# Kernel tuning notes

Hardware: AMD Instinct MI355X
Metric: run time of the kernel (lower is better)

## Reference

```python
import jax, jax.numpy as jnp
import numpy as np

B, N, DIM, IN_DIM, H = 8, 3136, 147, 64, 1
HD = IN_DIM // H          # per-head value/key dim = 64
MLP_HID = int(IN_DIM * 1.0)
EPS = 1e-5


def _ln(x, w, b):
    m = jnp.mean(x, axis=-1, keepdims=True)
    v = jnp.mean((x - m) ** 2, axis=-1, keepdims=True)
    return (x - m) / jnp.sqrt(v + EPS) * w + b


def setup_inputs() -> dict:
    key = jax.random.key(0)
    ks = jax.random.split(key, 12)
    r = lambda k, shp, s=0.02: (jax.random.normal(k, shp, dtype=jnp.float32) * s)
    return {
        "x": jax.random.normal(ks[0], (B, N, DIM), dtype=jnp.float32),
        "norm1_w": jnp.ones((DIM,), jnp.float32),
        "norm1_b": jnp.zeros((DIM,), jnp.float32),
        "qkv_w": r(ks[1], (3 * IN_DIM, DIM)),
        "scale": jnp.full((H,), (DIM // H) ** -0.5, dtype=jnp.float32),
        "proj_w": r(ks[2], (IN_DIM, IN_DIM)),
        "proj_b": jnp.zeros((IN_DIM,), jnp.float32),
        "norm2_w": jnp.ones((IN_DIM,), jnp.float32),
        "norm2_b": jnp.zeros((IN_DIM,), jnp.float32),
        "fc1_w": r(ks[3], (MLP_HID, IN_DIM)),
        "fc1_b": jnp.zeros((MLP_HID,), jnp.float32),
        "fc2_w": r(ks[4], (IN_DIM, MLP_HID)),
        "fc2_b": jnp.zeros((IN_DIM,), jnp.float32),
    }


def reference(x, norm1_w, norm1_b, qkv_w, scale, proj_w, proj_b,
              norm2_w, norm2_b, fc1_w, fc1_b, fc2_w, fc2_b):
    h = _ln(x, norm1_w, norm1_b)                               # [B,N,DIM]
    qkv = jnp.einsum('bnc,oc->bno', h, qkv_w)                  # [B,N,3*IN_DIM]
    qkv = qkv.reshape(B, N, 3, H, HD).transpose(2, 0, 3, 1, 4)  # [3,B,H,N,HD]
    q, k, v = qkv[0], qkv[1], qkv[2]
    # LMSA: learnable per-head scale + diagonal (self) exclusion mask
    attn = jnp.einsum('bhid,bhjd->bhij', q, k) * scale[None, :, None, None]
    eye = jnp.eye(N, dtype=bool)
    attn = jnp.where(eye[None, None], -jnp.inf, attn)
    attn = jax.nn.softmax(attn, axis=-1)
    o = jnp.einsum('bhij,bhjd->bhid', attn, v)                 # [B,H,N,HD]
    o = o.transpose(0, 2, 1, 3).reshape(B, N, IN_DIM)
    o = jnp.einsum('bnd,od->bno', o, proj_w) + proj_b
    # num_heads == 1 -> residual is v itself
    x_attn = v[:, 0] + o                                       # [B,N,IN_DIM]
    h2 = _ln(x_attn, norm2_w, norm2_b)
    h2 = jax.nn.gelu(jnp.einsum('bnd,hd->bnh', h2, fc1_w) + fc1_b,
                     approximate=False)
    h2 = jnp.einsum('bnh,oh->bno', h2, fc2_w) + fc2_b
    return x_attn + h2
```

## Files before the change

kernel.cpp:

```cpp
#include <hip/hip_runtime.h>
#include <math.h>
#include <stdint.h>

#define B_    8
#define N_    3136
#define DIM_  147
#define KP_   160
#define TOK_  (B_*N_)
#define QKV3_ 192
#define NSPLIT 4

typedef __attribute__((ext_vector_type(4)))  float f32x4;
typedef __attribute__((ext_vector_type(16))) float f32x16;
typedef __attribute__((ext_vector_type(4)))  unsigned int u32x4;
typedef __attribute__((ext_vector_type(2)))  unsigned int u32x2;
typedef __attribute__((ext_vector_type(8)))  short short8;
typedef float f32x4u __attribute__((ext_vector_type(4), aligned(4)));
typedef union { short8 s; u32x4 u; } pk8;

static __device__ __forceinline__ unsigned short f2b(float f){
  unsigned int u = __float_as_uint(f);
  u += 0x7fffu + ((u>>16)&1u);
  return (unsigned short)(u>>16);
}
static __device__ __forceinline__ unsigned int pk2(float a, float b){
  return ((unsigned int)f2b(b)<<16) | (unsigned int)f2b(a);
}
static __device__ __forceinline__ unsigned int pk2t(float a, float b){
  return (__float_as_uint(b) & 0xffff0000u) | (__float_as_uint(a)>>16);
}
static __device__ __forceinline__ float b2f(unsigned short s){
  return __uint_as_float(((unsigned int)s)<<16);
}

#define GLD16(gp, lp) __builtin_amdgcn_global_load_lds( \
    reinterpret_cast<const uint32_t __attribute__((address_space(1)))*>(reinterpret_cast<uintptr_t>(gp)), \
    reinterpret_cast<uint32_t __attribute__((address_space(3)))*>(reinterpret_cast<uintptr_t>(lp)), \
    16, 0, 0)

__global__ __launch_bounds__(256) void k_qkv(const float* __restrict__ x,
                                             const float* __restrict__ w1,
                                             const float* __restrict__ b1,
                                             const float* __restrict__ qkvw,
                                             const float* __restrict__ scale,
                                             unsigned short* __restrict__ qb,
                                             unsigned short* __restrict__ kb,
                                             unsigned short* __restrict__ vtb,
                                             unsigned short* __restrict__ vfb){
  __shared__ alignas(16) unsigned short Wb[192*168];
  unsigned short* A_ = Wb;
  unsigned short* VT = Wb;
  int tid = threadIdx.x;
  int w = tid>>6, lane = tid&63, quad = lane>>4, l16 = lane&15;
  int t0 = blockIdx.x*64;
  float sc2 = scale[0] * 1.44269504089f;

  #pragma unroll
  for(int half=0; half<2; half++){
    int g = half*32 + (tid>>3), e = tid&7;
    const float* xr = x + (size_t)(t0+g)*147;
    f32x4u xv[5];
    float s = 0.f, sq = 0.f;
    #pragma unroll
    for(int j=0;j<5;j++){
      int k = e + 8*j;
      int keff = (k > 36) ? 36 : k;
      f32x4u v = *(const f32x4u*)(xr + 4*keff);
      if(j == 4){
        v[0] = (k<=36) ? v[0] : 0.f;
        v[1] = (k<=36) ? v[1] : 0.f;
        v[2] = (k<=36) ? v[2] : 0.f;
        v[3] = (k< 36) ? v[3] : 0.f;
      }
      xv[j] = v;
      s  += (v[0]+v[1]) + (v[2]+v[3]);
      sq += (v[0]*v[0]+v[1]*v[1]) + (v[2]*v[2]+v[3]*v[3]);
    }
    s  += __shfl_xor(s,1,64);  s  += __shfl_xor(s,2,64);  s  += __shfl_xor(s,4,64);
    sq += __shfl_xor(sq,1,64); sq += __shfl_xor(sq,2,64); sq += __shfl_xor(sq,4,64);
    float mean = s*(1.f/147.f);
    float var  = sq*(1.f/147.f) - mean*mean;
    float rstd = rsqrtf(var + 1e-5f);
    #pragma unroll
    for(int j=0;j<5;j++){
      int k = e + 8*j;
      unsigned int lo = 0u, hi = 0u;
      if(k <= 36){
        int c0 = 4*k;
        int c3 = (k==36) ? 146 : c0+3;
        float y0 = (xv[j][0]-mean)*rstd*w1[c0]   + b1[c0];
        float y1 = (xv[j][1]-mean)*rstd*w1[c0+1] + b1[c0+1];
        float y2 = (xv[j][2]-mean)*rstd*w1[c0+2] + b1[c0+2];
        float y3 = (xv[j][3]-mean)*rstd*w1[c3]   + b1[c3];
        if(k == 36) y3 = 0.f;
        lo = pk2(y0,y1); hi = pk2(y2,y3);
      }
      *(u32x2*)(A_ + g*168 + 4*k) = (u32x2){lo,hi};
    }
  }
  __syncthreads();
  short8 Af[5];
  #pragma unroll
  for(int kk=0;kk<5;kk++)
    Af[kk] = *(const short8*)(A_ + (w*16+l16)*168 + kk*32 + quad*8);
  __syncthreads();
  {
    unsigned int* dst = (unsigned int*)Wb;
    #pragma unroll
    for(int rep=0; rep<15; rep++){
      int idx = rep*256 + tid;
      int row = idx/20, c = idx - row*20;
      u32x4 o = (u32x4){0u,0u,0u,0u};
      if(c < 19){
        const float* sp = qkvw + row*147 + c*8;
        f32x4u a = *(const f32x4u*)sp;
        o[0] = pk2(a[0],a[1]);
        if(c < 18){
          f32x4u bv = *(const f32x4u*)(sp+4);
          o[1] = pk2(a[2],a[3]);
          o[2] = pk2(bv[0],bv[1]);
          o[3] = pk2(bv[2],bv[3]);
        } else {
          o[1] = pk2(a[2],0.f);
        }
      }
      *(u32x4*)(dst + row*84 + c*4) = o;
    }
  }
  __syncthreads();
  f32x4 acc[12];
  #pragma unroll
  for(int i=0;i<12;i++) acc[i] = (f32x4){0.f,0.f,0.f,0.f};
  #pragma unroll
  for(int nt=0;nt<12;nt++){
    #pragma unroll
    for(int kk=0;kk<5;kk++){
      short8 Bf = *(const short8*)(Wb + (nt*16+l16)*168 + kk*32 + quad*8);
      acc[nt] = __builtin_amdgcn_mfma_f32_16x16x32_bf16(Af[kk], Bf, acc[nt], 0,0,0);
    }
  }
  #pragma unroll
  for(int nt=0;nt<12;nt++){
    int o = nt*16 + l16;
    #pragma unroll
    for(int r=0;r<4;r++){
      int tl = w*16 + quad*4 + r;
      int mg = t0 + tl;
      float val = acc[nt][r];
      if(o < 64)        qb[(size_t)mg*64 + o]        = f2b(val*sc2);
      else if(o < 128)  kb[(size_t)mg*64 + (o-64)]   = f2b(val);
      else              vfb[(size_t)mg*64 + (o-128)] = f2b(val);
    }
  }
  __syncthreads();
  #pragma unroll
  for(int nt=8;nt<12;nt++){
    int hd = (nt-8)*16 + l16;
    #pragma unroll
    for(int r=0;r<4;r++)
      VT[hd*72 + (w*16 + quad*4 + r)] = f2b(acc[nt][r]);
  }
  __syncthreads();
  {
    int b = t0 / N_, n0 = t0 - b*N_;
    const unsigned int* VT32 = (const unsigned int*)VT;
    unsigned int* vg = (unsigned int*)vtb + ((size_t)b*64)*(N_/2) + (n0>>1);
    #pragma unroll
    for(int rep=0;rep<8;rep++){
      int f = rep*256 + tid;
      int row = f>>5, c = f&31;
      vg[(size_t)row*(N_/2) + c] = VT32[row*36 + c];
    }
  }
}

__global__ __launch_bounds__(256,2) void k_attn(const unsigned short* __restrict__ qb,
                                                const unsigned short* __restrict__ kb,
                                                const unsigned short* __restrict__ vtb,
                                                unsigned short* __restrict__ Opart,
                                                float* __restrict__ lpart){
  __shared__ alignas(16) unsigned int L[8192];
  __shared__ float Lr[256];
  int tid = threadIdx.x;
  int s = tid>>6;
  int w2 = s>>1;
  int w  = s&1;
  int lane = tid&63;
  int h = lane>>5, l32 = lane&31, l7 = l32&7;
  int qt = blockIdx.x, sp = blockIdx.y, b = blockIdx.z;
  int qtile = 2*qt + w2;
  int live = (qtile < 49);
  int q0 = live ? qtile*64 : 0;
  int kv0 = (sp*49)>>2, kv1 = ((sp+1)*49)>>2;
  int nt = kv1 - kv0;

  short8 Qf[2][4];
  {
    const unsigned short* qg = qb + ((size_t)b*N_ + q0)*64;
    #pragma unroll
    for(int qh=0;qh<2;qh++)
      #pragma unroll
      for(int kc=0;kc<4;kc++)
        Qf[qh][kc] = *(const short8*)(qg + (32*qh + l32)*64 + 16*kc + 8*h);
  }
  int isK = (s < 2);
  int wh  = s & 1;
  int offG[4];
  {
    int pl = lane>>3, cl = lane&7;
    #pragma unroll
    for(int rr=0;rr<4;rr++){
      int p = rr*8 + pl;
      int cx = cl ^ (p&7);
      if(isK){
        int sig = (p & 0x13) | ((p&4)<<1) | ((p&8)>>1);
        offG[rr] = (32*wh + sig)*128 + cx*16;
      } else {
        offG[rr] = (32*wh + p)*(N_*2) + cx*16;
      }
    }
  }
  const char* sBase = isK ? ((const char*)kb  + (size_t)b*N_*128)
                          : ((const char*)vtb + (size_t)b*64*(size_t)(N_*2));
  int tileStride = isK ? 8192 : 128;
  int ldsOff = (isK ? 0 : 8192) + wh*4096;

  f32x16 O[2][2];
  #pragma unroll
  for(int qh=0;qh<2;qh++) for(int hdq=0;hdq<2;hdq++)
    #pragma unroll
    for(int r=0;r<16;r++) O[qh][hdq][r] = 0.f;
  float lracc[2][4];
  #pragma unroll
  for(int qh=0;qh<2;qh++)
    #pragma unroll
    for(int j=0;j<4;j++) lracc[qh][j] = 0.f;

  {
    const char* tp = sBase + (size_t)kv0*tileStride;
    #pragma unroll
    for(int rr=0;rr<4;rr++) GLD16(tp + offG[rr], (char*)L + ldsOff + rr*1024);
  }

  int cur = 0;
  for(int i=0;i<nt;i++){
    int kvt = kv0 + i;
    if(i+1 < nt){
      const char* tp = sBase + (size_t)(kvt+1)*tileStride;
      char* dst = (char*)L + (cur^1)*16384 + ldsOff;
      #pragma unroll
      for(int rr=0;rr<4;rr++) GLD16(tp + offG[rr], dst + rr*1024);
      asm volatile("s_waitcnt vmcnt(4)" ::: "memory");
    } else {
      asm volatile("s_waitcnt vmcnt(0)" ::: "memory");
    }
    __builtin_amdgcn_s_barrier();
    __builtin_amdgcn_sched_barrier(0);

    if(live){
      const unsigned short* Kh = (const unsigned short*)L + cur*8192 + w*2048;
      const unsigned short* Vh = (const unsigned short*)L + cur*8192 + 4096;

      short8 Kf[4];
      #pragma unroll
      for(int kc=0;kc<4;kc++)
        Kf[kc] = *(const short8*)(Kh + l32*64 + (((2*kc+h) ^ l7)&7)*8);
      #pragma unroll
      for(int qh=0;qh<2;qh++){
        f32x16 S;
        #pragma unroll
        for(int r=0;r<16;r++) S[r] = 0.f;
        #pragma unroll
        for(int kc=0;kc<4;kc++)
          S = __builtin_amdgcn_mfma_f32_32x32x16_bf16(Kf[kc], Qf[qh][kc], S, 0,0,0);
        f32x16 E;
        if(kvt == qtile){
          int dref = 32*qh + l32 - 32*w - 8*h;
          #pragma unroll
          for(int r=0;r<16;r++){
            int kvl = 16*((r>>3)&1) + 4*((r>>2)&1) + (r&3);
            float pv = (kvl == dref) ? 0.f : __builtin_amdgcn_exp2f(S[r]);
            E[r] = pv; lracc[qh][r&3] += pv;
          }
        } else {
          #pragma unroll
          for(int r=0;r<16;r++){
            float pv = __builtin_amdgcn_exp2f(S[r]);
            E[r] = pv; lracc[qh][r&3] += pv;
          }
        }
        pk8 Pb0, Pb1;
        Pb0.u = (u32x4){ pk2t(E[0],E[1]),   pk2t(E[2],E[3]),
                         pk2t(E[4],E[5]),   pk2t(E[6],E[7]) };
        Pb1.u = (u32x4){ pk2t(E[8],E[9]),   pk2t(E[10],E[11]),
                         pk2t(E[12],E[13]), pk2t(E[14],E[15]) };
        #pragma unroll
        for(int hdq=0;hdq<2;hdq++){
          short8 Vf0 = *(const short8*)(Vh + (32*hdq + l32)*64 + (((4*w + h) ^ l7)&7)*8);
          short8 Vf1 = *(const short8*)(Vh + (32*hdq + l32)*64 + (((4*w + 2 + h) ^ l7)&7)*8);
          O[qh][hdq] = __builtin_amdgcn_mfma_f32_32x32x16_bf16(Vf0, Pb0.s, O[qh][hdq], 0,0,0);
          O[qh][hdq] = __builtin_amdgcn_mfma_f32_32x32x16_bf16(Vf1, Pb1.s, O[qh][hdq], 0,0,0);
        }
      }
    }
    __builtin_amdgcn_sched_barrier(0);
    asm volatile("" ::: "memory");
    __builtin_amdgcn_s_barrier();
    cur ^= 1;
  }
  float lr[2];
  #pragma unroll
  for(int qh=0;qh<2;qh++)
    lr[qh] = (lracc[qh][0] + lracc[qh][1]) + (lracc[qh][2] + lracc[qh][3]);
  lr[0] += __shfl_xor(lr[0],32,64);
  lr[1] += __shfl_xor(lr[1],32,64);
  __syncthreads();
  unsigned int* Lp = L + w2*4096;
  float* Lrp = Lr + w2*128;
  if(w == 0){
    #pragma unroll
    for(int qh=0;qh<2;qh++)
      #pragma unroll
      for(int hdq=0;hdq<2;hdq++)
        #pragma unroll
        for(int r=0;r<16;r++)
          Lp[(qh*32 + hdq*16 + r)*64 + lane] = __float_as_uint(O[qh][hdq][r]);
    Lrp[lane]      = lr[0];
    Lrp[64 + lane] = lr[1];
  }
  __syncthreads();
  if(w == 1){
    #pragma unroll
    for(int qh=0;qh<2;qh++)
      #pragma unroll
      for(int hdq=0;hdq<2;hdq++)
        #pragma unroll
        for(int r=0;r<16;r++)
          O[qh][hdq][r] += __uint_as_float(Lp[(qh*32 + hdq*16 + r)*64 + lane]);
    float lt0 = lr[0] + Lrp[lane];
    float lt1 = lr[1] + Lrp[64 + lane];
    size_t lb = (size_t)sp*TOK_ + (size_t)b*N_ + q0;
    if(live && lane < 32){ lpart[lb + lane] = lt0; lpart[lb + 32 + lane] = lt1; }
    #pragma unroll
    for(int qh=0;qh<2;qh++){
      int q = 32*qh + l32;
      #pragma unroll
      for(int hdq=0;hdq<2;hdq++)
        #pragma unroll
        for(int k2=0;k2<8;k2++){
          int idx = 16*hdq + 4*(k2>>1) + 2*h + (k2&1);
          Lp[q*36 + idx] = pk2(O[qh][hdq][2*k2], O[qh][hdq][2*k2+1]);
        }
    }
    if(live){
      unsigned int* og = (unsigned int*)(Opart + ((size_t)sp*TOK_ + (size_t)b*N_ + q0)*64);
      #pragma unroll
      for(int rep=0;rep<8;rep++){
        int f = rep*64 + lane;
        int row = f>>3, c4 = f&7;
        *(u32x4*)(og + row*32 + c4*4) = *(const u32x4*)&Lp[row*36 + c4*4];
      }
    }
  }
}

__global__ __launch_bounds__(256) void k_mlp(const unsigned short* __restrict__ Opart,
                                             const float* __restrict__ lpart,
                                             const unsigned short* __restrict__ vfb,
                                             const float* __restrict__ projw,
                                             const float* __restrict__ fc1w,
                                             const float* __restrict__ fc2w,
                                             const float* __restrict__ projb,
                                             const float* __restrict__ n2w,
                                             const float* __restrict__ n2b,
                                             const float* __restrict__ fc1b,
                                             const float* __restrict__ fc2b,
                                             float* __restrict__ out){
  __shared__ alignas(16) unsigned short Ws[3][64*72];
  __shared__ alignas(16) unsigned short Xs[64*72];
  unsigned int* Xs32 = (unsigned int*)Xs;
  int tid = threadIdx.x;
  int w = tid>>6, lane = tid&63, quad = lane>>4, l16 = lane&15;
  int t0 = blockIdx.x*64;

  {
    #pragma unroll
    for(int rep=0;rep<2;rep++){
      int f = rep*256 + tid;
      int row = f>>3, c = f&7;
      int so = (row<<6) + (c<<3);
      f32x4 a0 = *(const f32x4*)(projw + so), b0 = *(const f32x4*)(projw + so + 4);
      f32x4 a1 = *(const f32x4*)(fc1w  + so), b1v = *(const f32x4*)(fc1w  + so + 4);
      f32x4 a2 = *(const f32x4*)(fc2w  + so), b2 = *(const f32x4*)(fc2w  + so + 4);
      *(u32x4*)((unsigned int*)Ws[0] + row*36 + c*4) =
        (u32x4){pk2(a0[0],a0[1]),pk2(a0[2],a0[3]),pk2(b0[0],b0[1]),pk2(b0[2],b0[3])};
      *(u32x4*)((unsigned int*)Ws[1] + row*36 + c*4) =
        (u32x4){pk2(a1[0],a1[1]),pk2(a1[2],a1[3]),pk2(b1v[0],b1v[1]),pk2(b1v[2],b1v[3])};
      *(u32x4*)((unsigned int*)Ws[2] + row*36 + c*4) =
        (u32x4){pk2(a2[0],a2[1]),pk2(a2[2],a2[3]),pk2(b2[0],b2[1]),pk2(b2[2],b2[3])};
    }
  }
  #pragma unroll
  for(int i=0;i<2;i++){
    int f = i*256 + tid;
    int row = f>>3, c = f&7;
    float lo[4] = {0,0,0,0}, hi[4] = {0,0,0,0};
    float lsum = 0.f;
    #pragma unroll
    for(int s=0;s<NSPLIT;s++){
      u32x4 a = *((const u32x4*)(Opart + ((size_t)s*TOK_ + t0)*64) + row*8 + c);
      #pragma unroll
      for(int k=0;k<4;k++){
        lo[k] += __uint_as_float(a[k]<<16);
        hi[k] += __uint_as_float(a[k] & 0xffff0000u);
      }
      lsum += lpart[(size_t)s*TOK_ + t0 + row];
    }
    float linv = 1.f/lsum;
    u32x4 o;
    #pragma unroll
    for(int k=0;k<4;k++) o[k] = pk2(lo[k]*linv, hi[k]*linv);
    *(u32x4*)&Xs32[row*36 + c*4] = o;
  }
  __syncthreads();

  short8 Af[2];
  #pragma unroll
  for(int kk=0;kk<2;kk++)
    Af[kk] = *(const short8*)(Xs + (w*16+l16)*72 + kk*32 + quad*8);
  f32x4 acc[4];
  #pragma unroll
  for(int i=0;i<4;i++) acc[i] = (f32x4){0.f,0.f,0.f,0.f};
  #pragma unroll
  for(int jt=0;jt<4;jt++)
    #pragma unroll
    for(int kk=0;kk<2;kk++){
      short8 Bf = *(const short8*)(Ws[0] + (jt*16+l16)*72 + kk*32 + quad*8);
      acc[jt] = __builtin_amdgcn_mfma_f32_16x16x32_bf16(Af[kk], Bf, acc[jt], 0,0,0);
    }
  float xa[4][4];
  #pragma unroll
  for(int jt=0;jt<4;jt++){
    int col = jt*16 + l16;
    float pb = projb[col];
    #pragma unroll
    for(int r=0;r<4;r++){
      int tg = t0 + w*16 + quad*4 + r;
      xa[jt][r] = acc[jt][r] + pb + b2f(vfb[(size_t)tg*64 + col]);
    }
  }
  #pragma unroll
  for(int r=0;r<4;r++){
    float s = 0.f, sq = 0.f;
    #pragma unroll
    for(int jt=0;jt<4;jt++){ s += xa[jt][r]; sq += xa[jt][r]*xa[jt][r]; }
    s  += __shfl_xor(s,1,64);  s  += __shfl_xor(s,2,64);
    s  += __shfl_xor(s,4,64);  s  += __shfl_xor(s,8,64);
    sq += __shfl_xor(sq,1,64); sq += __shfl_xor(sq,2,64);
    sq += __shfl_xor(sq,4,64); sq += __shfl_xor(sq,8,64);
    float mu = s*(1.f/64.f);
    float var = sq*(1.f/64.f) - mu*mu;
    float rstd = rsqrtf(var + 1e-5f);
    #pragma unroll
    for(int jt=0;jt<4;jt++){
      int col = jt*16 + l16;
      Xs[(w*16+quad*4+r)*72 + col] = f2b((xa[jt][r]-mu)*rstd*n2w[col] + n2b[col]);
    }
  }
  #pragma unroll
  for(int kk=0;kk<2;kk++)
    Af[kk] = *(const short8*)(Xs + (w*16+l16)*72 + kk*32 + quad*8);
  f32x4 acc2[4];
  #pragma unroll
  for(int i=0;i<4;i++) acc2[i] = (f32x4){0.f,0.f,0.f,0.f};
  #pragma unroll
  for(int jt=0;jt<4;jt++)
    #pragma unroll
    for(int kk=0;kk<2;kk++){
      short8 Bf = *(const short8*)(Ws[1] + (jt*16+l16)*72 + kk*32 + quad*8);
      acc2[jt] = __builtin_amdgcn_mfma_f32_16x16x32_bf16(Af[kk], Bf, acc2[jt], 0,0,0);
    }
  #pragma unroll
  for(int jt=0;jt<4;jt++){
    int col = jt*16 + l16;
    float fb = fc1b[col];
    #pragma unroll
    for(int r=0;r<4;r++){
      float g = acc2[jt][r] + fb;
      float z = g*0.70710678118f;
      float az = fabsf(z);
      float t = 1.f/(1.f + 0.3275911f*az);
      float poly = ((((1.061405429f*t - 1.453152027f)*t + 1.421413741f)*t - 0.284496736f)*t + 0.254829592f)*t;
      float er = 1.f - poly*__builtin_amdgcn_exp2f(-az*az*1.44269504089f);
      er = (z < 0.f) ? -er : er;
      Xs[(w*16+quad*4+r)*72 + col] = f2b(0.5f*g*(1.f + er));
    }
  }
  #pragma unroll
  for(int kk=0;kk<2;kk++)
    Af[kk] = *(const short8*)(Xs + (w*16+l16)*72 + kk*32 + quad*8);
  f32x4 acc3[4];
  #pragma unroll
  for(int i=0;i<4;i++) acc3[i] = (f32x4){0.f,0.f,0.f,0.f};
  #pragma unroll
  for(int jt=0;jt<4;jt++)
    #pragma unroll
    for(int kk=0;kk<2;kk++){
      short8 Bf = *(const short8*)(Ws[2] + (jt*16+l16)*72 + kk*32 + quad*8);
      acc3[jt] = __builtin_amdgcn_mfma_f32_16x16x32_bf16(Af[kk], Bf, acc3[jt], 0,0,0);
    }
  #pragma unroll
  for(int jt=0;jt<4;jt++){
    int col = jt*16 + l16;
    float ob2 = fc2b[col];
    #pragma unroll
    for(int r=0;r<4;r++){
      int tg = t0 + w*16 + quad*4 + r;
      out[(size_t)tg*64 + col] = xa[jt][r] + acc3[jt][r] + ob2;
    }
  }
}

extern "C" void kernel_launch(void* const* d_in, const int* in_sizes, int n_in,
                              void* d_out, int out_size, void* d_ws, size_t ws_size,
                              hipStream_t stream){
  const float* x     = (const float*)d_in[0];
  const float* n1w   = (const float*)d_in[1];
  const float* n1b   = (const float*)d_in[2];
  const float* qkvw  = (const float*)d_in[3];
  const float* scale = (const float*)d_in[4];
  const float* projw = (const float*)d_in[5];
  const float* projb = (const float*)d_in[6];
  const float* n2w   = (const float*)d_in[7];
  const float* n2b   = (const float*)d_in[8];
  const float* fc1w  = (const float*)d_in[9];
  const float* fc1b  = (const float*)d_in[10];
  const float* fc2w  = (const float*)d_in[11];
  const float* fc2b  = (const float*)d_in[12];

  char* base = (char*)d_ws;
  unsigned short* qb  = (unsigned short*)(base + 0);
  unsigned short* kb  = (unsigned short*)(base + 3211264);
  unsigned short* vtb = (unsigned short*)(base + 6422528);
  unsigned short* vfb = (unsigned short*)(base + 9633792);
  unsigned short* Op  = (unsigned short*)(base + 12845056);
  float*          lp  = (float*)(base + 25690112);

  hipLaunchKernelGGL(k_qkv,  dim3(TOK_/64),    dim3(256), 0, stream,
                     x, n1w, n1b, qkvw, scale, qb, kb, vtb, vfb);
  hipLaunchKernelGGL(k_attn, dim3(25,NSPLIT,8), dim3(256), 0, stream, qb, kb, vtb, Op, lp);
  hipLaunchKernelGGL(k_mlp,  dim3(TOK_/64),    dim3(256), 0, stream, Op, lp, vfb,
                     projw, fc1w, fc2w, projb, n2w, n2b, fc1b, fc2b, (float*)d_out);
}
```

Baseline: 144.6 us.

## Deepen attention K/V prefetch to a 4-stage LDS ring with one barrier per tile

Grows the LDS K/V staging area from a double buffer to a four-slot ring and keeps three tiles in flight, with vmcnt waits adjusted to the pipeline depth. It also removes the trailing barrier in each loop iteration, since the slot being refilled is three tiles ahead. The aim is to hide global-load latency better and cut synchronisation. LDS use rises to 64KB per block, which may lower occupancy below the two blocks per CU requested by launch bounds.

```diff
diff --git a/kernel.cpp b/kernel.cpp
--- a/kernel.cpp
+++ b/kernel.cpp
@@ -179,7 +179,7 @@
                                                 const unsigned short* __restrict__ vtb,
                                                 unsigned short* __restrict__ Opart,
                                                 float* __restrict__ lpart){
-  __shared__ alignas(16) unsigned int L[8192];
+  __shared__ alignas(16) char LB[65536];
   __shared__ float Lr[256];
   int tid = threadIdx.x;
   int s = tid>>6;
@@ -225,6 +225,12 @@
   int tileStride = isK ? 8192 : 128;
   int ldsOff = (isK ? 0 : 8192) + wh*4096;
 
+#define STAGE(BUFI, T) { \
+    const char* tp_ = sBase + (size_t)(T)*tileStride; \
+    char* db_ = LB + (BUFI)*16384 + ldsOff; \
+    _Pragma("unroll") \
+    for(int rr=0;rr<4;rr++) GLD16(tp_ + offG[rr], db_ + rr*1024); }
+
   f32x16 O[2][2];
   #pragma unroll
   for(int qh=0;qh<2;qh++) for(int hdq=0;hdq<2;hdq++)
@@ -236,30 +242,23 @@
     #pragma unroll
     for(int j=0;j<4;j++) lracc[qh][j] = 0.f;
 
-  {
-    const char* tp = sBase + (size_t)kv0*tileStride;
-    #pragma unroll
-    for(int rr=0;rr<4;rr++) GLD16(tp + offG[rr], (char*)L + ldsOff + rr*1024);
-  }
-
-  int cur = 0;
+  STAGE(0, kv0);
+  STAGE(1, kv0+1);
+  STAGE(2, kv0+2);
+
   for(int i=0;i<nt;i++){
     int kvt = kv0 + i;
-    if(i+1 < nt){
-      const char* tp = sBase + (size_t)(kvt+1)*tileStride;
-      char* dst = (char*)L + (cur^1)*16384 + ldsOff;
-      #pragma unroll
-      for(int rr=0;rr<4;rr++) GLD16(tp + offG[rr], dst + rr*1024);
-      asm volatile("s_waitcnt vmcnt(4)" ::: "memory");
-    } else {
-      asm volatile("s_waitcnt vmcnt(0)" ::: "memory");
-    }
+    if(i <= nt-3)      { asm volatile("s_waitcnt vmcnt(8)" ::: "memory"); }
+    else if(i == nt-2) { asm volatile("s_waitcnt vmcnt(4)" ::: "memory"); }
+    else               { asm volatile("s_waitcnt vmcnt(0)" ::: "memory"); }
     __builtin_amdgcn_s_barrier();
     __builtin_amdgcn_sched_barrier(0);
+    if(i+3 < nt) STAGE((i+3)&3, kvt+3);
 
     if(live){
-      const unsigned short* Kh = (const unsigned short*)L + cur*8192 + w*2048;
-      const unsigned short* Vh = (const unsigned short*)L + cur*8192 + 4096;
+      const char* cb = LB + (i&3)*16384;
+      const unsigned short* Kh = (const unsigned short*)cb + w*2048;
+      const unsigned short* Vh = (const unsigned short*)cb + 4096;
 
       short8 Kf[4];
       #pragma unroll
@@ -304,10 +303,9 @@
       }
     }
     __builtin_amdgcn_sched_barrier(0);
-    asm volatile("" ::: "memory");
-    __builtin_amdgcn_s_barrier();
-    cur ^= 1;
-  }
+  }
+#undef STAGE
+
   float lr[2];
   #pragma unroll
   for(int qh=0;qh<2;qh++)
@@ -315,7 +313,7 @@
   lr[0] += __shfl_xor(lr[0],32,64);
   lr[1] += __shfl_xor(lr[1],32,64);
   __syncthreads();
-  unsigned int* Lp = L + w2*4096;
+  unsigned int* Lp = (unsigned int*)LB + w2*4096;
   float* Lrp = Lr + w2*128;
   if(w == 0){
     #pragma unroll
```

Result: no change. 143.7 us (-0.6%).
